# Kernel tuning notes

Hardware: AMD Instinct MI355X
Metric: run time of the kernel (lower is better)

The kernel has to match this reference:

```python
import jax, jax.numpy as jnp
import numpy as np

EPS = 1e-9
NUM_HEADS = 16
D = 1024      # input_dim == hidden_dim
B, S = 2, 2048


def layer_norm(x, scale, shift):
    mu = x.mean(axis=-1, keepdims=True)
    # torch std is unbiased (ddof=1); eps added to std, not variance
    std = jnp.std(x, axis=-1, ddof=1, keepdims=True)
    return scale * (x - mu) / (std + EPS) + shift


def setup_inputs() -> dict:
    key = jax.random.key(0)
    ks = jax.random.split(key, 18)
    d, h = D, D
    w = lambda k, sh: jax.random.normal(k, sh, dtype=jnp.float32) * 0.02
    return {
        "inputs": jax.random.normal(ks[0], (B, S, d), dtype=jnp.float32),
        "ln1_scale": jax.random.normal(ks[1], (d,), dtype=jnp.float32),
        "ln1_shift": jax.random.normal(ks[2], (d,), dtype=jnp.float32),
        "Wq": w(ks[3], (d, h)), "bq": jnp.zeros((h,), jnp.float32),
        "Wk": w(ks[4], (d, h)), "bk": jnp.zeros((h,), jnp.float32),
        "Wv": w(ks[5], (d, h)), "bv": jnp.zeros((h,), jnp.float32),
        "Wo": w(ks[6], (h, d)), "bo": jnp.zeros((d,), jnp.float32),
        "W1": w(ks[7], (d, 4 * d)), "b1": jnp.zeros((4 * d,), jnp.float32),
        "W2": w(ks[8], (4 * d, d)), "b2": jnp.zeros((d,), jnp.float32),
        "ln2_scale": jax.random.normal(ks[9], (d,), dtype=jnp.float32),
        "ln2_shift": jax.random.normal(ks[10], (d,), dtype=jnp.float32),
    }


def mhsa(x, Wq, bq, Wk, bk, Wv, bv, Wo, bo):
    b, s, d = x.shape
    nh, dh = NUM_HEADS, D // NUM_HEADS
    q = (x @ Wq + bq).reshape(b, s, nh, dh).transpose(0, 2, 1, 3)  # b h s d
    k = (x @ Wk + bk).reshape(b, s, nh, dh).transpose(0, 2, 1, 3)
    v = (x @ Wv + bv).reshape(b, s, nh, dh).transpose(0, 2, 1, 3)
    scores = jnp.einsum("bhqd,bhkd->bhqk", q, k) / jnp.sqrt(jnp.float32(dh))
    causal = jnp.triu(jnp.ones((s, s), dtype=bool), k=1)  # mask above diagonal
    scores = jnp.where(causal, -jnp.inf, scores)
    p = jax.nn.softmax(scores, axis=-1)
    p = jnp.where(jnp.isnan(p), 0.0, p)  # NaN-fill as in original
    out = jnp.einsum("bhqk,bhkd->bhqd", p, v)
    out = out.transpose(0, 2, 1, 3).reshape(b, s, nh * dh)
    return out @ Wo + bo


def reference(inputs, ln1_scale, ln1_shift, Wq, bq, Wk, bk, Wv, bv, Wo, bo,
              W1, b1, W2, b2, ln2_scale, ln2_shift):
    o1 = layer_norm(inputs, ln1_scale, ln1_shift)
    o1 = mhsa(o1, Wq, bq, Wk, bk, Wv, bv, Wo, bo) + inputs
    o2 = layer_norm(o1, ln2_scale, ln2_shift)
    # NOTE: original adds the residual from the *normalized* tensor, not o1
    ffn = jax.nn.relu(o2 @ W1 + b1) @ W2 + b2
    return ffn + o2
```

## Files before the change

kernel.cpp:

```cpp
#include <hip/hip_runtime.h>
#include <hip/hip_bf16.h>
#include <math.h>

#define BB 2
#define SS 2048
#define DD 1024
#define HH 16
#define DH 64
#define NROW (BB*SS)
#define FFN (4*DD)

typedef __attribute__((ext_vector_type(8))) __bf16 bf16x8;
typedef __attribute__((ext_vector_type(4))) __bf16 bf16x4;
typedef __attribute__((ext_vector_type(4))) float f32x4;

#define QSCALE 0.18033688011112042f

__device__ __forceinline__ ushort f2b(float f) {
    union { float f; uint32_t u; } x; x.f = f;
    uint32_t r = x.u + 0x7FFF + ((x.u >> 16) & 1);
    return (ushort)(r >> 16);
}
__device__ __forceinline__ float b2f(ushort u) {
    union { uint32_t u; float f; } x; x.u = (uint32_t)u << 16;
    return x.f;
}

__global__ __launch_bounds__(256)
void ln_kernel(const float* __restrict__ x, const float* __restrict__ scale,
               const float* __restrict__ shift, ushort* __restrict__ y) {
    int row = blockIdx.x;
    const float* xr = x + (size_t)row * DD;
    ushort* yr = y + (size_t)row * DD;
    int t = threadIdx.x;
    float v[4];
    float s = 0.f, ss = 0.f;
#pragma unroll
    for (int i = 0; i < 4; ++i) {
        v[i] = xr[t + 256 * i];
        s += v[i];
        ss += v[i] * v[i];
    }
#pragma unroll
    for (int off = 32; off; off >>= 1) {
        s  += __shfl_xor(s, off);
        ss += __shfl_xor(ss, off);
    }
    __shared__ float red[8];
    int w = t >> 6;
    if ((t & 63) == 0) { red[w] = s; red[w + 4] = ss; }
    __syncthreads();
    float st  = red[0] + red[1] + red[2] + red[3];
    float sst = red[4] + red[5] + red[6] + red[7];
    float mu = st * (1.f / DD);
    float var = (sst - DD * mu * mu) * (1.f / (DD - 1));
    var = fmaxf(var, 0.f);
    float inv = 1.f / (sqrtf(var) + 1e-9f);
#pragma unroll
    for (int i = 0; i < 4; ++i) {
        int c = t + 256 * i;
        yr[c] = f2b(scale[c] * (v[i] - mu) * inv + shift[c]);
    }
}

__global__ __launch_bounds__(256)
void ln_res_kernel(const ushort* __restrict__ xa, const float* __restrict__ xb,
                   const float* __restrict__ scale, const float* __restrict__ shift,
                   ushort* __restrict__ yb) {
    int row = blockIdx.x;
    const ushort* ar = xa + (size_t)row * DD;
    const float* br = xb + (size_t)row * DD;
    ushort* ybr = yb + (size_t)row * DD;
    int t = threadIdx.x;
    float v[4];
    float s = 0.f, ss = 0.f;
#pragma unroll
    for (int i = 0; i < 4; ++i) {
        int c = t + 256 * i;
        v[i] = b2f(ar[c]) + br[c];
        s += v[i];
        ss += v[i] * v[i];
    }
#pragma unroll
    for (int off = 32; off; off >>= 1) {
        s  += __shfl_xor(s, off);
        ss += __shfl_xor(ss, off);
    }
    __shared__ float red[8];
    int w = t >> 6;
    if ((t & 63) == 0) { red[w] = s; red[w + 4] = ss; }
    __syncthreads();
    float st  = red[0] + red[1] + red[2] + red[3];
    float sst = red[4] + red[5] + red[6] + red[7];
    float mu = st * (1.f / DD);
    float var = (sst - DD * mu * mu) * (1.f / (DD - 1));
    var = fmaxf(var, 0.f);
    float inv = 1.f / (sqrtf(var) + 1e-9f);
#pragma unroll
    for (int i = 0; i < 4; ++i) {
        int c = t + 256 * i;
        ybr[c] = f2b(scale[c] * (v[i] - mu) * inv + shift[c]);
    }
}

__global__ __launch_bounds__(256)
void transpose_bf16_kernel(const float* __restrict__ W, ushort* __restrict__ Wt,
                           int K, int N) {
    __shared__ ushort tile[32][33];
    int tx = threadIdx.x & 31;
    int ty = threadIdx.x >> 5;
    int n0 = blockIdx.x * 32;
    int k0 = blockIdx.y * 32;
#pragma unroll
    for (int i = 0; i < 32; i += 8)
        tile[ty + i][tx] = f2b(W[(size_t)(k0 + ty + i) * N + n0 + tx]);
    __syncthreads();
#pragma unroll
    for (int i = 0; i < 32; i += 8)
        Wt[(size_t)(n0 + ty + i) * K + k0 + tx] = tile[tx][ty + i];
}

__global__ __launch_bounds__(256)
void transpose4_bf16_kernel(const float* __restrict__ W0, const float* __restrict__ W1,
                            const float* __restrict__ W2, const float* __restrict__ W3,
                            ushort* __restrict__ Wt) {
    __shared__ ushort tile[32][33];
    int z = blockIdx.z;
    const float* W = z == 0 ? W0 : (z == 1 ? W1 : (z == 2 ? W2 : W3));
    ushort* dst = Wt + (size_t)z * DD * DD;
    int tx = threadIdx.x & 31;
    int ty = threadIdx.x >> 5;
    int n0 = blockIdx.x * 32;
    int k0 = blockIdx.y * 32;
#pragma unroll
    for (int i = 0; i < 32; i += 8)
        tile[ty + i][tx] = f2b(W[(size_t)(k0 + ty + i) * DD + n0 + tx]);
    __syncthreads();
#pragma unroll
    for (int i = 0; i < 32; i += 8)
        dst[(size_t)(n0 + ty + i) * DD + k0 + tx] = tile[tx][ty + i];
}

__global__ __launch_bounds__(256)
void reduce_wo_kernel(const ushort* __restrict__ p, const float* __restrict__ bias,
                      ushort* __restrict__ yb) {
    const size_t MN = (size_t)NROW * DD;
    int i = (blockIdx.x * 256 + threadIdx.x) * 4;
    ushort4 a = *reinterpret_cast<const ushort4*>(p + i);
    ushort4 b = *reinterpret_cast<const ushort4*>(p + MN + i);
    ushort4 c4 = *reinterpret_cast<const ushort4*>(p + 2 * MN + i);
    ushort4 d4 = *reinterpret_cast<const ushort4*>(p + 3 * MN + i);
    int c = i & (DD - 1);
    float4 bs = *reinterpret_cast<const float4*>(bias + c);
    ushort4 o;
    o.x = f2b(b2f(a.x) + b2f(b.x) + b2f(c4.x) + b2f(d4.x) + bs.x);
    o.y = f2b(b2f(a.y) + b2f(b.y) + b2f(c4.y) + b2f(d4.y) + bs.y);
    o.z = f2b(b2f(a.z) + b2f(b.z) + b2f(c4.z) + b2f(d4.z) + bs.z);
    o.w = f2b(b2f(a.w) + b2f(b.w) + b2f(c4.w) + b2f(d4.w) + bs.w);
    *reinterpret_cast<ushort4*>(yb + i) = o;
}

__global__ __launch_bounds__(256)
void reduce_ffn2_kernel(const ushort* __restrict__ p, const float* __restrict__ bias,
                        const ushort* __restrict__ res, float* __restrict__ out) {
    const size_t MN = (size_t)NROW * DD;
    int i = (blockIdx.x * 256 + threadIdx.x) * 4;
    ushort4 a = *reinterpret_cast<const ushort4*>(p + i);
    ushort4 b = *reinterpret_cast<const ushort4*>(p + MN + i);
    ushort4 c4 = *reinterpret_cast<const ushort4*>(p + 2 * MN + i);
    ushort4 d4 = *reinterpret_cast<const ushort4*>(p + 3 * MN + i);
    ushort4 r = *reinterpret_cast<const ushort4*>(res + i);
    int c = i & (DD - 1);
    float4 bs = *reinterpret_cast<const float4*>(bias + c);
    float4 o;
    o.x = b2f(a.x) + b2f(b.x) + b2f(c4.x) + b2f(d4.x) + bs.x + b2f(r.x);
    o.y = b2f(a.y) + b2f(b.y) + b2f(c4.y) + b2f(d4.y) + bs.y + b2f(r.y);
    o.z = b2f(a.z) + b2f(b.z) + b2f(c4.z) + b2f(d4.z) + bs.z + b2f(r.z);
    o.w = b2f(a.w) + b2f(b.w) + b2f(c4.w) + b2f(d4.w) + bs.w + b2f(r.w);
    *reinterpret_cast<float4*>(out + i) = o;
}

#define GBM 128
#define GBK 32

template <int MODE, bool BF16_OUT, int DEPTH, int BN>
__global__ __launch_bounds__(512)
void gemm_bf16_kernel(const ushort* __restrict__ A, const ushort* __restrict__ Wt,
                      const float* __restrict__ bias, const ushort* __restrict__ addsrc,
                      void* __restrict__ Cout, int M, int N, int K, int lda,
                      const float* __restrict__ bias2, const float* __restrict__ bias3,
                      void* __restrict__ out2, void* __restrict__ out3) {
    __shared__ ushort As[DEPTH][GBM * GBK];
    __shared__ ushort Bs[DEPTH][BN * GBK];
    constexpr int NF = BN / 64;

    int tid = threadIdx.x;
    int lane = tid & 63;
    int wid = tid >> 6;
    int wr = wid >> 2, wc = wid & 3;

    int gx = gridDim.x;
    int nwg = gx * gridDim.y;
    int orig = blockIdx.y * gx + blockIdx.x;
    int q8 = nwg >> 3;
    int swz = (orig & 7) * q8 + (orig >> 3);
    int bx = swz % gx, by = swz / gx;

    int brow = by * GBM;
    int bcol = bx * BN;
    size_t koff = (size_t)blockIdx.z * K;

    int lrow = lane & 15;
    int kgrp = lane >> 4;

    f32x4 acc[4][NF] = {};

    auto stage = [&](int buf, int k0) {
        {
            int row = tid >> 2;
            int gran = (tid & 3) ^ ((row >> 1) & 3);
            const char* ga = (const char*)A +
                ((size_t)(brow + row) * lda + koff + k0) * 2 + gran * 16;
            __builtin_amdgcn_global_load_lds(
                (const __attribute__((address_space(1))) uint32_t*)ga,
                (__attribute__((address_space(3))) uint32_t*)(&As[buf][0] + (wid * 16) * GBK),
                16, 0, 0);
        }
#pragma unroll
        for (int i = 0; i < BN / 128; ++i) {
            int idx = i * 512 + tid;
            int row = idx >> 2;
            int gran = (idx & 3) ^ ((row >> 1) & 3);
            const char* gb = (const char*)Wt +
                ((size_t)(bcol + row) * lda + koff + k0) * 2 + gran * 16;
            __builtin_amdgcn_global_load_lds(
                (const __attribute__((address_space(1))) uint32_t*)gb,
                (__attribute__((address_space(3))) uint32_t*)(&Bs[buf][0] + (i * 128 + wid * 16) * GBK),
                16, 0, 0);
        }
    };

    int nk = K / GBK;
    constexpr int PRE = DEPTH - 1;
#pragma unroll
    for (int s = 0; s < PRE; ++s)
        if (s < nk) stage(s, s * GBK);

    int cur = 0, stg = PRE;
    for (int t = 0; t < nk; ++t) {
        __builtin_amdgcn_sched_barrier(0);
        int rem = nk - 1 - t;
        if constexpr (DEPTH == 5 && BN == 128) {
            if (rem >= 3)      asm volatile("s_waitcnt vmcnt(6)" ::: "memory");
            else if (rem == 2) asm volatile("s_waitcnt vmcnt(4)" ::: "memory");
            else if (rem == 1) asm volatile("s_waitcnt vmcnt(2)" ::: "memory");
            else               asm volatile("s_waitcnt vmcnt(0)" ::: "memory");
        } else if constexpr (DEPTH == 3 && BN == 128) {
            if (rem >= 1)      asm volatile("s_waitcnt vmcnt(2)" ::: "memory");
            else               asm volatile("s_waitcnt vmcnt(0)" ::: "memory");
        } else if constexpr (DEPTH == 3 && BN == 256) {
            if (rem >= 1)      asm volatile("s_waitcnt vmcnt(3)" ::: "memory");
            else               asm volatile("s_waitcnt vmcnt(0)" ::: "memory");
        } else {
            asm volatile("s_waitcnt vmcnt(0)" ::: "memory");
        }
        asm volatile("s_barrier" ::: "memory");
        if (t + PRE < nk) stage(stg, (t + PRE) * GBK);

        bf16x8 afrag[4], bfrag[NF];
#pragma unroll
        for (int mi = 0; mi < 4; ++mi) {
            int row = wr * 64 + mi * 16 + lrow;
            int gran = kgrp ^ ((row >> 1) & 3);
            afrag[mi] = *(const bf16x8*)((const char*)&As[cur][0] + row * 64 + gran * 16);
        }
#pragma unroll
        for (int ni = 0; ni < NF; ++ni) {
            int row = wc * (BN / 4) + ni * 16 + lrow;
            int gran = kgrp ^ ((row >> 1) & 3);
            bfrag[ni] = *(const bf16x8*)((const char*)&Bs[cur][0] + row * 64 + gran * 16);
        }
#pragma unroll
        for (int mi = 0; mi < 4; ++mi)
#pragma unroll
            for (int ni = 0; ni < NF; ++ni)
                acc[mi][ni] = __builtin_amdgcn_mfma_f32_16x16x32_bf16(
                    afrag[mi], bfrag[ni], acc[mi][ni], 0, 0, 0);

        cur = (cur == DEPTH - 1) ? 0 : cur + 1;
        stg = (stg == DEPTH - 1) ? 0 : stg + 1;
    }

    if (MODE == 3) {
        int which = bcol >> 10;
        const float* bs = which == 0 ? bias : (which == 1 ? bias2 : bias3);
#pragma unroll
        for (int ni = 0; ni < NF; ++ni) {
            int col = bcol + wc * (BN / 4) + ni * 16 + lrow;
            int lcol = col & 1023;
            float bsv = bs[lcol];
#pragma unroll
            for (int mi = 0; mi < 4; ++mi) {
                f32x4 a = acc[mi][ni];
#pragma unroll
                for (int j = 0; j < 4; ++j) {
                    int row = brow + wr * 64 + mi * 16 + kgrp * 4 + j;
                    float val = a[j] + bsv;
                    if (which == 2) {
                        size_t idx = (size_t)(row >> 11) * ((size_t)DD * SS)
                                   + (size_t)lcol * SS + (row & (SS - 1));
                        ((ushort*)out3)[idx] = f2b(val);
                    } else if (which == 0) {
                        ((ushort*)Cout)[(size_t)row * DD + lcol] = f2b(val * QSCALE);
                    } else {
                        ((ushort*)out2)[(size_t)row * DD + lcol] = f2b(val);
                    }
                }
            }
        }
        return;
    }

    if (MODE == 4) {
        ushort* dst = (ushort*)Cout + (size_t)blockIdx.z * ((size_t)M * N);
#pragma unroll
        for (int ni = 0; ni < NF; ++ni) {
            int col = bcol + wc * (BN / 4) + ni * 16 + lrow;
#pragma unroll
            for (int mi = 0; mi < 4; ++mi) {
                f32x4 a = acc[mi][ni];
#pragma unroll
                for (int j = 0; j < 4; ++j) {
                    int row = brow + wr * 64 + mi * 16 + kgrp * 4 + j;
                    dst[(size_t)row * N + col] = f2b(a[j]);
                }
            }
        }
        return;
    }

#pragma unroll
    for (int ni = 0; ni < NF; ++ni) {
        int col = bcol + wc * (BN / 4) + ni * 16 + lrow;
        float bsv = bias[col];
#pragma unroll
        for (int mi = 0; mi < 4; ++mi) {
            f32x4 a = acc[mi][ni];
#pragma unroll
            for (int j = 0; j < 4; ++j) {
                int row = brow + wr * 64 + mi * 16 + kgrp * 4 + j;
                float val = a[j] + bsv;
                if (MODE == 1) val = fmaxf(val, 0.f);
                if (BF16_OUT)
                    ((ushort*)Cout)[(size_t)row * N + col] = f2b(val);
                else
                    ((float*)Cout)[(size_t)row * N + col] = val;
            }
        }
    }
}

__global__ __launch_bounds__(256)
void attn_mfma_kernel(const ushort* __restrict__ Qg, const ushort* __restrict__ Kg,
                      const ushort* __restrict__ Vtg, ushort* __restrict__ Og) {
    __shared__ ushort Qs[64 * 64];
    __shared__ ushort Ks[2][64 * 64];
    __shared__ ushort Vs[2][64 * 64];

    int tid = threadIdx.x;
    int lane = tid & 63;
    int wid = tid >> 6;
    int bh = blockIdx.x;
    int b = bh >> 4, h = bh & 15;
    int y = blockIdx.y;
    int jj = y >> 3, kk = y & 7;
    int qt = jj * 8 + ((jj & 1) ? 7 - kk : kk);
    int q0 = qt * 64;

    const ushort* Qbase = Qg + ((size_t)(b * SS + q0)) * DD + h * DH;
    const ushort* Kbase = Kg + ((size_t)(b * SS)) * DD + h * DH;
    const ushort* Vbase = Vtg + (size_t)bh * DH * SS;

    int r0 = wid * 16;
    int rr0 = r0 + (lane >> 3);
    int g0 = lane & 7;
    int g = lane >> 4;
    int lr = lane & 15;

    auto stageKV = [&](int buf, int k0) {
#pragma unroll
        for (int i = 0; i < 2; ++i) {
            int rr = rr0 + i * 8;
            int gg = g0 ^ (rr & 7);
            const ushort* srck = Kbase + (size_t)(k0 + rr) * DD + gg * 8;
            __builtin_amdgcn_global_load_lds(
                (const __attribute__((address_space(1))) uint32_t*)srck,
                (__attribute__((address_space(3))) uint32_t*)(&Ks[buf][0] + (r0 + i * 8) * 64),
                16, 0, 0);
            const ushort* srcv = Vbase + (size_t)rr * SS + k0 + gg * 8;
            __builtin_amdgcn_global_load_lds(
                (const __attribute__((address_space(1))) uint32_t*)srcv,
                (__attribute__((address_space(3))) uint32_t*)(&Vs[buf][0] + (r0 + i * 8) * 64),
                16, 0, 0);
        }
    };

    int nt = q0 / 64 + 1;

    {
#pragma unroll
        for (int i = 0; i < 2; ++i) {
            int rr = rr0 + i * 8;
            int gg = g0 ^ (rr & 7);
            const ushort* src = Qbase + (size_t)rr * DD + gg * 8;
            __builtin_amdgcn_global_load_lds(
                (const __attribute__((address_space(1))) uint32_t*)src,
                (__attribute__((address_space(3))) uint32_t*)(Qs + (r0 + i * 8) * 64),
                16, 0, 0);
        }
    }
    stageKV(0, 0);
    asm volatile("s_waitcnt vmcnt(4)" ::: "memory");

    bf16x8 aq[2];
    {
        int r = wid * 16 + lr;
#pragma unroll
        for (int ks = 0; ks < 2; ++ks) {
            int lg = ks * 4 + g;
            aq[ks] = *(const bf16x8*)((const char*)Qs + r * 128 + ((lg ^ (r & 7)) << 4));
        }
    }
    ushort* Ps = Qs;

    f32x4 oacc[4] = {};
    float m = -INFINITY, l = 0.f;
    const float THR = 11.0f;
    int qa = q0 + wid * 16 + lr;

    int cur = 0;
    for (int t = 0; t < nt; ++t) {
        __builtin_amdgcn_sched_barrier(0);
        asm volatile("s_waitcnt vmcnt(0)" ::: "memory");
        asm volatile("s_barrier" ::: "memory");
        if (t + 1 < nt) stageKV(cur ^ 1, (t + 1) * 64);
        int k0 = t * 64;

        f32x4 sacc[4] = {};
        __builtin_amdgcn_s_setprio(1);
#pragma unroll
        for (int ni = 0; ni < 4; ++ni) {
            int r = ni * 16 + lr;
#pragma unroll
            for (int ks = 0; ks < 2; ++ks) {
                int lg = ks * 4 + g;
                bf16x8 bk = *(const bf16x8*)((const char*)&Ks[cur][0] + r * 128 + ((lg ^ (r & 7)) << 4));
                sacc[ni] = __builtin_amdgcn_mfma_f32_16x16x32_bf16(bk, aq[ks], sacc[ni], 0, 0, 0);
            }
        }
        __builtin_amdgcn_s_setprio(0);

        if (k0 == q0) {
#pragma unroll
            for (int ni = 0; ni < 4; ++ni) {
#pragma unroll
                for (int j = 0; j < 4; ++j) {
                    int key = q0 + ni * 16 + g * 4 + j;
                    if (key > qa) sacc[ni][j] = -INFINITY;
                }
            }
        }

        float mx = sacc[0][0];
#pragma unroll
        for (int ni = 0; ni < 4; ++ni)
#pragma unroll
            for (int j = 0; j < 4; ++j) mx = fmaxf(mx, sacc[ni][j]);
        mx = fmaxf(mx, __shfl_xor(mx, 16));
        mx = fmaxf(mx, __shfl_xor(mx, 32));

        if (__any(mx > m + THR)) {
            float mn = fmaxf(m, mx);
            float corr = __builtin_amdgcn_exp2f(m - mn);
            m = mn;
            l *= corr;
            float cj[4];
#pragma unroll
            for (int j = 0; j < 4; ++j)
                cj[j] = __shfl(corr, (lane & 48) | (g * 4 + j));
#pragma unroll
            for (int ni = 0; ni < 4; ++ni)
#pragma unroll
                for (int j = 0; j < 4; ++j) oacc[ni][j] *= cj[j];
        }

        float p[4][4];
        float rs = 0.f;
#pragma unroll
        for (int ni = 0; ni < 4; ++ni)
#pragma unroll
            for (int j = 0; j < 4; ++j) {
                p[ni][j] = __builtin_amdgcn_exp2f(sacc[ni][j] - m);
                rs += p[ni][j];
            }
        rs += __shfl_xor(rs, 16);
        rs += __shfl_xor(rs, 32);
        l += rs;

        {
            int row = wid * 16 + lr;
#pragma unroll
            for (int ni = 0; ni < 4; ++ni) {
                bf16x4 w4 = { (__bf16)p[ni][0], (__bf16)p[ni][1],
                              (__bf16)p[ni][2], (__bf16)p[ni][3] };
                int gran = (ni * 2 + (g >> 1)) ^ (row & 7);
                *(bf16x4*)((char*)Ps + row * 128 + (gran << 4) + (g & 1) * 8) = w4;
            }
        }
        asm volatile("s_waitcnt lgkmcnt(0)" ::: "memory");

        bf16x8 ap[2];
        {
            int r = wid * 16 + lr;
#pragma unroll
            for (int ks = 0; ks < 2; ++ks) {
                int lg = ks * 4 + g;
                ap[ks] = *(const bf16x8*)((const char*)Ps + r * 128 + ((lg ^ (r & 7)) << 4));
            }
        }
        __builtin_amdgcn_s_setprio(1);
#pragma unroll
        for (int ni = 0; ni < 4; ++ni) {
            int r = ni * 16 + lr;
#pragma unroll
            for (int ks = 0; ks < 2; ++ks) {
                int lg = ks * 4 + g;
                bf16x8 bv = *(const bf16x8*)((const char*)&Vs[cur][0] + r * 128 + ((lg ^ (r & 7)) << 4));
                oacc[ni] = __builtin_amdgcn_mfma_f32_16x16x32_bf16(ap[ks], bv, oacc[ni], 0, 0, 0);
            }
        }
        __builtin_amdgcn_s_setprio(0);
        cur ^= 1;
    }

#pragma unroll
    for (int j = 0; j < 4; ++j) {
        float lj = __shfl(l, (lane & 48) | (g * 4 + j));
        float inv = 1.f / lj;
        int gr = q0 + wid * 16 + g * 4 + j;
#pragma unroll
        for (int ni = 0; ni < 4; ++ni) {
            int d = ni * 16 + lr;
            Og[((size_t)(b * SS + gr)) * DD + h * DH + d] = f2b(oacc[ni][j] * inv);
        }
    }
}

extern "C" void kernel_launch(void* const* d_in, const int* in_sizes, int n_in,
                              void* d_out, int out_size, void* d_ws, size_t ws_size,
                              hipStream_t stream) {
    const float* inputs    = (const float*)d_in[0];
    const float* ln1_scale = (const float*)d_in[1];
    const float* ln1_shift = (const float*)d_in[2];
    const float* Wq = (const float*)d_in[3];
    const float* bq = (const float*)d_in[4];
    const float* Wk = (const float*)d_in[5];
    const float* bk = (const float*)d_in[6];
    const float* Wv = (const float*)d_in[7];
    const float* bv = (const float*)d_in[8];
    const float* Wo = (const float*)d_in[9];
    const float* bo = (const float*)d_in[10];
    const float* W1 = (const float*)d_in[11];
    const float* b1 = (const float*)d_in[12];
    const float* W2 = (const float*)d_in[13];
    const float* b2 = (const float*)d_in[14];
    const float* ln2_scale = (const float*)d_in[15];
    const float* ln2_shift = (const float*)d_in[16];
    float* out = (float*)d_out;

    const size_t MB = 1024 * 1024;
    char* w = (char*)d_ws;
    ushort* q_b   = (ushort*)(w + 0 * MB);
    ushort* k_b   = (ushort*)(w + 8 * MB);
    ushort* vt_b  = (ushort*)(w + 16 * MB);
    ushort* att_b = (ushort*)(w + 24 * MB);
    ushort* pw    = (ushort*)(w + 32 * MB);
    ushort* proj_b= (ushort*)(w + 0 * MB);
    ushort* o2_b  = (ushort*)(w + 8 * MB);
    ushort* pf    = (ushort*)(w + 16 * MB);
    ushort* h1_b  = (ushort*)(w + 64 * MB);
    ushort* wq_t  = (ushort*)(w + 96 * MB);
    ushort* wk_t  = (ushort*)(w + 98 * MB);
    ushort* wv_t  = (ushort*)(w + 100 * MB);
    ushort* wo_t  = (ushort*)(w + 102 * MB);
    ushort* w1_t  = (ushort*)(w + 104 * MB);
    ushort* w2_t  = (ushort*)(w + 112 * MB);
    ushort* xn_b  = (ushort*)(w + 120 * MB);

    transpose4_bf16_kernel<<<dim3(DD / 32, DD / 32, 4), 256, 0, stream>>>(
        Wq, Wk, Wv, Wo, wq_t);
    transpose_bf16_kernel<<<dim3(FFN / 32, DD / 32), 256, 0, stream>>>(W1, w1_t, DD, FFN);
    transpose_bf16_kernel<<<dim3(DD / 32, FFN / 32), 256, 0, stream>>>(W2, w2_t, FFN, DD);

    ln_kernel<<<NROW, 256, 0, stream>>>(inputs, ln1_scale, ln1_shift, xn_b);

    dim3 gqkv(3 * DD / 128, NROW / GBM, 1);
    gemm_bf16_kernel<3, true, 3, 128><<<gqkv, 512, 0, stream>>>(
        xn_b, wq_t, bq, nullptr, q_b, NROW, 3 * DD, DD, DD, bk, bv, k_b, vt_b);

    dim3 ga(BB * HH, SS / 64);
    attn_mfma_kernel<<<ga, 256, 0, stream>>>(q_b, k_b, vt_b, att_b);

    dim3 gwo(DD / 256, NROW / GBM, 4);
    gemm_bf16_kernel<4, false, 3, 256><<<gwo, 512, 0, stream>>>(
        att_b, wo_t, nullptr, nullptr, pw, NROW, DD, DD / 4, DD, nullptr, nullptr, nullptr, nullptr);
    reduce_wo_kernel<<<(NROW * DD / 4) / 256, 256, 0, stream>>>(pw, bo, proj_b);

    ln_res_kernel<<<NROW, 256, 0, stream>>>(proj_b, inputs, ln2_scale, ln2_shift, o2_b);

    dim3 g2(FFN / 256, NROW / GBM, 1);
    gemm_bf16_kernel<1, true, 3, 256><<<g2, 512, 0, stream>>>(
        o2_b, w1_t, b1, nullptr, h1_b, NROW, FFN, DD, DD, nullptr, nullptr, nullptr, nullptr);

    dim3 gf2(DD / 256, NROW / GBM, 4);
    gemm_bf16_kernel<4, false, 3, 256><<<gf2, 512, 0, stream>>>(
        h1_b, w2_t, nullptr, nullptr, pf, NROW, DD, FFN / 4, FFN, nullptr, nullptr, nullptr, nullptr);
    reduce_ffn2_kernel<<<(NROW * DD / 4) / 256, 256, 0, stream>>>(pf, b2, o2_b, out);
}
```

Before: 231.7 us.

## Widen attention blocks to 128 query rows sharing K/V tiles across 8 waves

The attention kernel now launches 512-thread blocks that each cover 128 query rows instead of 64. All eight waves share each staged 64-key K/V tile, which halves the global-to-LDS K/V traffic per query and lets each lane issue one load per matrix instead of two. The causal mask is now computed per wave, so the lower-half waves run one extra, fully masked tile. LDS swizzled offsets are also precomputed once outside the loop rather than recomputed every iteration. The costs are fewer, larger blocks (half the grid), the wasted masked tile, and a different causal load-balancing order.

```diff
diff --git a/kernel.cpp b/kernel.cpp
--- a/kernel.cpp
+++ b/kernel.cpp
@@ -360,10 +360,10 @@
     }
 }
 
-__global__ __launch_bounds__(256)
+__global__ __launch_bounds__(512)
 void attn_mfma_kernel(const ushort* __restrict__ Qg, const ushort* __restrict__ Kg,
                       const ushort* __restrict__ Vtg, ushort* __restrict__ Og) {
-    __shared__ ushort Qs[64 * 64];
+    __shared__ ushort Qs[128 * 64];
     __shared__ ushort Ks[2][64 * 64];
     __shared__ ushort Vs[2][64 * 64];
 
@@ -373,41 +373,35 @@
     int bh = blockIdx.x;
     int b = bh >> 4, h = bh & 15;
     int y = blockIdx.y;
-    int jj = y >> 3, kk = y & 7;
-    int qt = jj * 8 + ((jj & 1) ? 7 - kk : kk);
-    int q0 = qt * 64;
-
-    const ushort* Qbase = Qg + ((size_t)(b * SS + q0)) * DD + h * DH;
+    int pr = (y < 8) ? y : 23 - y;
+    int qp0 = pr * 128;
+    int nt = (qp0 >> 6) + 2;
+
+    const ushort* Qbase = Qg + ((size_t)(b * SS + qp0)) * DD + h * DH;
     const ushort* Kbase = Kg + ((size_t)(b * SS)) * DD + h * DH;
     const ushort* Vbase = Vtg + (size_t)bh * DH * SS;
 
-    int r0 = wid * 16;
-    int rr0 = r0 + (lane >> 3);
-    int g0 = lane & 7;
     int g = lane >> 4;
     int lr = lane & 15;
 
     auto stageKV = [&](int buf, int k0) {
-#pragma unroll
-        for (int i = 0; i < 2; ++i) {
-            int rr = rr0 + i * 8;
-            int gg = g0 ^ (rr & 7);
-            const ushort* srck = Kbase + (size_t)(k0 + rr) * DD + gg * 8;
-            __builtin_amdgcn_global_load_lds(
-                (const __attribute__((address_space(1))) uint32_t*)srck,
-                (__attribute__((address_space(3))) uint32_t*)(&Ks[buf][0] + (r0 + i * 8) * 64),
-                16, 0, 0);
-            const ushort* srcv = Vbase + (size_t)rr * SS + k0 + gg * 8;
-            __builtin_amdgcn_global_load_lds(
-                (const __attribute__((address_space(1))) uint32_t*)srcv,
-                (__attribute__((address_space(3))) uint32_t*)(&Vs[buf][0] + (r0 + i * 8) * 64),
-                16, 0, 0);
-        }
+        int rr = wid * 8 + (lane >> 3);
+        int gg = (lane & 7) ^ (rr & 7);
+        const ushort* srck = Kbase + (size_t)(k0 + rr) * DD + gg * 8;
+        __builtin_amdgcn_global_load_lds(
+            (const __attribute__((address_space(1))) uint32_t*)srck,
+            (__attribute__((address_space(3))) uint32_t*)(&Ks[buf][0] + (wid * 8) * 64),
+            16, 0, 0);
+        const ushort* srcv = Vbase + (size_t)rr * SS + k0 + gg * 8;
+        __builtin_amdgcn_global_load_lds(
+            (const __attribute__((address_space(1))) uint32_t*)srcv,
+            (__attribute__((address_space(3))) uint32_t*)(&Vs[buf][0] + (wid * 8) * 64),
+            16, 0, 0);
     };
 
-    int nt = q0 / 64 + 1;
-
     {
+        int rr0 = wid * 16 + (lane >> 3);
+        int g0 = lane & 7;
 #pragma unroll
         for (int i = 0; i < 2; ++i) {
             int rr = rr0 + i * 8;
@@ -415,28 +409,42 @@
             const ushort* src = Qbase + (size_t)rr * DD + gg * 8;
             __builtin_amdgcn_global_load_lds(
                 (const __attribute__((address_space(1))) uint32_t*)src,
-                (__attribute__((address_space(3))) uint32_t*)(Qs + (r0 + i * 8) * 64),
+                (__attribute__((address_space(3))) uint32_t*)(Qs + (wid * 16 + i * 8) * 64),
                 16, 0, 0);
         }
     }
     stageKV(0, 0);
-    asm volatile("s_waitcnt vmcnt(4)" ::: "memory");
+    asm volatile("s_waitcnt vmcnt(2)" ::: "memory");
+
+    int offF[8];
+#pragma unroll
+    for (int ni = 0; ni < 4; ++ni)
+#pragma unroll
+        for (int ks = 0; ks < 2; ++ks) {
+            int r = ni * 16 + lr;
+            offF[ni * 2 + ks] = r * 128 + (((ks * 4 + g) ^ (r & 7)) << 4);
+        }
+    int rq = wid * 16 + lr;
+    int offQ[2];
+#pragma unroll
+    for (int ks = 0; ks < 2; ++ks)
+        offQ[ks] = rq * 128 + (((ks * 4 + g) ^ (rq & 7)) << 4);
+    int offPw[4];
+#pragma unroll
+    for (int ni = 0; ni < 4; ++ni)
+        offPw[ni] = rq * 128 + (((ni * 2 + (g >> 1)) ^ (rq & 7)) << 4) + (g & 1) * 8;
 
     bf16x8 aq[2];
-    {
-        int r = wid * 16 + lr;
-#pragma unroll
-        for (int ks = 0; ks < 2; ++ks) {
-            int lg = ks * 4 + g;
-            aq[ks] = *(const bf16x8*)((const char*)Qs + r * 128 + ((lg ^ (r & 7)) << 4));
-        }
-    }
+#pragma unroll
+    for (int ks = 0; ks < 2; ++ks)
+        aq[ks] = *(const bf16x8*)((const char*)Qs + offQ[ks]);
     ushort* Ps = Qs;
 
     f32x4 oacc[4] = {};
     float m = -INFINITY, l = 0.f;
     const float THR = 11.0f;
-    int qa = q0 + wid * 16 + lr;
+    int qa = qp0 + wid * 16 + lr;
+    int qw0 = qp0 + wid * 16;
 
     int cur = 0;
     for (int t = 0; t < nt; ++t) {
@@ -449,23 +457,20 @@
         f32x4 sacc[4] = {};
         __builtin_amdgcn_s_setprio(1);
 #pragma unroll
-        for (int ni = 0; ni < 4; ++ni) {
-            int r = ni * 16 + lr;
+        for (int ni = 0; ni < 4; ++ni)
 #pragma unroll
             for (int ks = 0; ks < 2; ++ks) {
-                int lg = ks * 4 + g;
-                bf16x8 bk = *(const bf16x8*)((const char*)&Ks[cur][0] + r * 128 + ((lg ^ (r & 7)) << 4));
+                bf16x8 bk = *(const bf16x8*)((const char*)&Ks[cur][0] + offF[ni * 2 + ks]);
                 sacc[ni] = __builtin_amdgcn_mfma_f32_16x16x32_bf16(bk, aq[ks], sacc[ni], 0, 0, 0);
             }
-        }
         __builtin_amdgcn_s_setprio(0);
 
-        if (k0 == q0) {
+        if (k0 + 63 > qw0) {
 #pragma unroll
             for (int ni = 0; ni < 4; ++ni) {
 #pragma unroll
                 for (int j = 0; j < 4; ++j) {
-                    int key = q0 + ni * 16 + g * 4 + j;
+                    int key = k0 + ni * 16 + g * 4 + j;
                     if (key > qa) sacc[ni][j] = -INFINITY;
                 }
             }
@@ -507,38 +512,26 @@
         rs += __shfl_xor(rs, 32);
         l += rs;
 
-        {
-            int row = wid * 16 + lr;
-#pragma unroll
-            for (int ni = 0; ni < 4; ++ni) {
-                bf16x4 w4 = { (__bf16)p[ni][0], (__bf16)p[ni][1],
-                              (__bf16)p[ni][2], (__bf16)p[ni][3] };
-                int gran = (ni * 2 + (g >> 1)) ^ (row & 7);
-                *(bf16x4*)((char*)Ps + row * 128 + (gran << 4) + (g & 1) * 8) = w4;
-            }
+#pragma unroll
+        for (int ni = 0; ni < 4; ++ni) {
+            bf16x4 w4 = { (__bf16)p[ni][0], (__bf16)p[ni][1],
+                          (__bf16)p[ni][2], (__bf16)p[ni][3] };
+            *(bf16x4*)((char*)Ps + offPw[ni]) = w4;
         }
         asm volatile("s_waitcnt lgkmcnt(0)" ::: "memory");
 
         bf16x8 ap[2];
-        {
-            int r = wid * 16 + lr;
+#pragma unroll
+        for (int ks = 0; ks < 2; ++ks)
+            ap[ks] = *(const bf16x8*)((const char*)Ps + offQ[ks]);
+        __builtin_amdgcn_s_setprio(1);
+#pragma unroll
+        for (int ni = 0; ni < 4; ++ni)
 #pragma unroll
             for (int ks = 0; ks < 2; ++ks) {
-                int lg = ks * 4 + g;
-                ap[ks] = *(const bf16x8*)((const char*)Ps + r * 128 + ((lg ^ (r & 7)) << 4));
-            }
-        }
-        __builtin_amdgcn_s_setprio(1);
-#pragma unroll
-        for (int ni = 0; ni < 4; ++ni) {
-            int r = ni * 16 + lr;
-#pragma unroll
-            for (int ks = 0; ks < 2; ++ks) {
-                int lg = ks * 4 + g;
-                bf16x8 bv = *(const bf16x8*)((const char*)&Vs[cur][0] + r * 128 + ((lg ^ (r & 7)) << 4));
+                bf16x8 bv = *(const bf16x8*)((const char*)&Vs[cur][0] + offF[ni * 2 + ks]);
                 oacc[ni] = __builtin_amdgcn_mfma_f32_16x16x32_bf16(ap[ks], bv, oacc[ni], 0, 0, 0);
             }
-        }
         __builtin_amdgcn_s_setprio(0);
         cur ^= 1;
     }
@@ -547,7 +540,7 @@
     for (int j = 0; j < 4; ++j) {
         float lj = __shfl(l, (lane & 48) | (g * 4 + j));
         float inv = 1.f / lj;
-        int gr = q0 + wid * 16 + g * 4 + j;
+        int gr = qp0 + wid * 16 + g * 4 + j;
 #pragma unroll
         for (int ni = 0; ni < 4; ++ni) {
             int d = ni * 16 + lr;
@@ -608,8 +601,8 @@
     gemm_bf16_kernel<3, true, 3, 128><<<gqkv, 512, 0, stream>>>(
         xn_b, wq_t, bq, nullptr, q_b, NROW, 3 * DD, DD, DD, bk, bv, k_b, vt_b);
 
-    dim3 ga(BB * HH, SS / 64);
-    attn_mfma_kernel<<<ga, 256, 0, stream>>>(q_b, k_b, vt_b, att_b);
+    dim3 ga(BB * HH, SS / 128);
+    attn_mfma_kernel<<<ga, 512, 0, stream>>>(q_b, k_b, vt_b, att_b);
 
     dim3 gwo(DD / 256, NROW / GBM, 4);
     gemm_bf16_kernel<4, false, 3, 256><<<gwo, 512, 0, stream>>>(
```

New measurement: 233.6 us. Within noise of the previous version (+0.8%).
